# Performance work log

Hardware: AMD Instinct MI355X
Metric: run time of the kernel (lower is better)

Reference implementation:

```python
import jax, jax.numpy as jnp
import numpy as np

NUM_BINS = 256


def setup_inputs() -> dict:
    key = jax.random.key(0)
    x = jax.random.uniform(key, (16, 3, 1024, 1024), dtype=jnp.float32)
    return {"x": x}


def reference(x) -> jnp.ndarray:
    B, C, H, W = x.shape
    # Quantize to NUM_BINS levels (values in [0,1] so truncation == torch .long())
    x_flat = jnp.clip(x, 0.0, 1.0).reshape(B, C, H * W)
    x_q = jnp.clip((x_flat * (NUM_BINS - 1)).astype(jnp.int32), 0, NUM_BINS - 1)
    # Per-(B,C) histogram via a single flat scatter-add: offset each (b,c)
    # slice into its own NUM_BINS-wide segment of one 1-D buffer.
    offsets = (jnp.arange(B * C, dtype=jnp.int32) * NUM_BINS).reshape(B, C, 1)
    flat_idx = (x_q + offsets).reshape(-1)
    hist = jnp.zeros(B * C * NUM_BINS, dtype=jnp.float32).at[flat_idx].add(1.0)
    hist = hist.reshape(B, C, NUM_BINS)
    # CDF, normalized by total count (clamped at 1 to avoid div-by-zero)
    cdf = jnp.cumsum(hist, axis=2)
    cdf = cdf / jnp.maximum(cdf[:, :, -1:], 1.0)
    # Remap each pixel through its channel's CDF
    y_flat = jnp.take_along_axis(cdf, x_q, axis=2)
    return y_flat.reshape(B, C, H, W).astype(x.dtype)
```

## Files before the change

### kernel.cpp

```cpp
#include <hip/hip_runtime.h>

#define NB 256
#define NCH 48
#define HW (1024*1024)
#define WPC (HW / 4)
#define BPC 32
#define GRID (NCH * BPC)
#define THREADS 256
#define KTOT 32
#define KLDS 6
#define KREG (KTOT - KLDS)
#define FB_BPC 64

__device__ __forceinline__ int quant255(float v) {
    v = fminf(fmaxf(v, 0.0f), 1.0f);
    int q = (int)(v * 255.0f);
    q = q < 0 ? 0 : q;
    q = q > 255 ? 255 : q;
    return q;
}

__device__ __forceinline__ unsigned quant_pack(float4 v, unsigned* lh, int w) {
    int q0 = quant255(v.x), q1 = quant255(v.y);
    int q2 = quant255(v.z), q3 = quant255(v.w);
    atomicAdd(&lh[w * NB + q0], 1u);
    atomicAdd(&lh[w * NB + q1], 1u);
    atomicAdd(&lh[w * NB + q2], 1u);
    atomicAdd(&lh[w * NB + q3], 1u);
    return (unsigned)q0 | ((unsigned)q1 << 8)
         | ((unsigned)q2 << 16) | ((unsigned)q3 << 24);
}

__global__ __launch_bounds__(THREADS, 6) void fused_he_kernel(
    const float* __restrict__ x, unsigned int* __restrict__ ghist,
    unsigned int* __restrict__ bar, float* __restrict__ y) {
    __shared__ unsigned int sq[KLDS * THREADS];
    __shared__ unsigned int lh[4 * NB];

    const int t  = threadIdx.x;
    const int w  = t >> 6;
    const int ch  = blockIdx.x / BPC;
    const int blk = blockIdx.x % BPC;

    for (int i = t; i < 4 * NB; i += THREADS) lh[i] = 0u;
    __syncthreads();

    const float4* xp = (const float4*)x + (size_t)ch * WPC
                       + (size_t)blk * (KTOT * THREADS);

    for (int k = 0; k < KLDS; ++k) {
        float4 v = xp[k * THREADS + t];
        sq[k * THREADS + t] = quant_pack(v, lh, w);
    }
    unsigned int qpk[KREG];
    #pragma unroll
    for (int k = 0; k < KREG; ++k) {
        float4 v = xp[(KLDS + k) * THREADS + t];
        qpk[k] = quant_pack(v, lh, w);
    }
    __syncthreads();

    unsigned int s = lh[t] + lh[NB + t] + lh[2 * NB + t] + lh[3 * NB + t];
    atomicAdd(&ghist[ch * NB + t], s);
    __threadfence();
    __syncthreads();

    if (t == 0) {
        atomicAdd(bar, 1u);
        while (atomicAdd(bar, 0u) < (unsigned)GRID)
            __builtin_amdgcn_s_sleep(8);
    }
    __syncthreads();

    float* sbuf = (float*)lh;
    float* lut  = (float*)lh + NB;
    sbuf[t] = (float)atomicAdd(&ghist[ch * NB + t], 0u);
    __syncthreads();
    for (int off = 1; off < NB; off <<= 1) {
        float add = (t >= off) ? sbuf[t - off] : 0.0f;
        __syncthreads();
        sbuf[t] += add;
        __syncthreads();
    }
    float total = sbuf[NB - 1];
    lut[t] = sbuf[t] / fmaxf(total, 1.0f);
    __syncthreads();

    float4* yp = (float4*)y + (size_t)ch * WPC + (size_t)blk * (KTOT * THREADS);
    for (int k = 0; k < KLDS; ++k) {
        unsigned p = sq[k * THREADS + t];
        yp[k * THREADS + t] = make_float4(lut[p & 255], lut[(p >> 8) & 255],
                                          lut[(p >> 16) & 255], lut[p >> 24]);
    }
    #pragma unroll
    for (int k = 0; k < KREG; ++k) {
        unsigned p = qpk[k];
        yp[(KLDS + k) * THREADS + t] = make_float4(lut[p & 255], lut[(p >> 8) & 255],
                                                   lut[(p >> 16) & 255], lut[p >> 24]);
    }
}

__global__ __launch_bounds__(THREADS) void hist_quant_kernel(
    const float* __restrict__ x, unsigned int* __restrict__ ghist,
    unsigned int* __restrict__ q) {
    __shared__ unsigned int lh[4 * NB];
    const int t = threadIdx.x;
    const int w = t >> 6;
    for (int i = t; i < 4 * NB; i += THREADS) lh[i] = 0u;
    __syncthreads();

    const int ch  = blockIdx.x / FB_BPC;
    const int blk = blockIdx.x % FB_BPC;
    const float4* xp = (const float4*)(x + (size_t)ch * HW);
    unsigned int* qp = q + (size_t)ch * WPC;
    const int n4 = WPC / FB_BPC;
    const int base = blk * n4;

    for (int i = base + t; i < base + n4; i += THREADS) {
        float4 v = xp[i];
        qp[i] = quant_pack(v, lh, w);
    }
    __syncthreads();
    unsigned int s = lh[t] + lh[NB + t] + lh[2 * NB + t] + lh[3 * NB + t];
    if (s) atomicAdd(&ghist[ch * NB + t], s);
}

__global__ __launch_bounds__(THREADS) void cdf_remap_kernel(
    const unsigned int* __restrict__ q, const unsigned int* __restrict__ ghist,
    float* __restrict__ y) {
    __shared__ float sbuf[NB];
    __shared__ float lut[NB];
    const int t = threadIdx.x;
    const int ch  = blockIdx.x / FB_BPC;
    const int blk = blockIdx.x % FB_BPC;

    sbuf[t] = (float)ghist[ch * NB + t];
    __syncthreads();
    for (int off = 1; off < NB; off <<= 1) {
        float add = (t >= off) ? sbuf[t - off] : 0.0f;
        __syncthreads();
        sbuf[t] += add;
        __syncthreads();
    }
    float total = sbuf[NB - 1];
    lut[t] = sbuf[t] / fmaxf(total, 1.0f);
    __syncthreads();

    const unsigned int* qp = q + (size_t)ch * WPC;
    float4*             yp = (float4*)(y + (size_t)ch * HW);
    const int n4 = WPC / FB_BPC;
    const int base = blk * n4;
    for (int i = base + t; i < base + n4; i += THREADS) {
        unsigned p = qp[i];
        yp[i] = make_float4(lut[p & 255], lut[(p >> 8) & 255],
                            lut[(p >> 16) & 255], lut[p >> 24]);
    }
}

extern "C" void kernel_launch(void* const* d_in, const int* in_sizes, int n_in,
                              void* d_out, int out_size, void* d_ws, size_t ws_size,
                              hipStream_t stream) {
    const float* x = (const float*)d_in[0];
    float* y = (float*)d_out;

    unsigned int* ghist = (unsigned int*)d_ws;
    unsigned int* bar   = (unsigned int*)((char*)d_ws + 60 * 1024);
    unsigned int* q     = (unsigned int*)((char*)d_ws + 256 * 1024);

    hipMemsetAsync(d_ws, 0, 64 * 1024, stream);

    int occ = 0;
    hipError_t qe = hipOccupancyMaxActiveBlocksPerMultiprocessor(
        &occ, fused_he_kernel, THREADS, 0);
    bool fused_ok = (qe == hipSuccess) && (occ >= GRID / 256);

    if (fused_ok) {
        fused_he_kernel<<<GRID, THREADS, 0, stream>>>(x, ghist, bar, y);
    } else {
        hist_quant_kernel<<<NCH * FB_BPC, THREADS, 0, stream>>>(x, ghist, q);
        cdf_remap_kernel <<<NCH * FB_BPC, THREADS, 0, stream>>>(q, ghist, y);
    }
}
```

Before: 368.6 us.

## Replace persistent grid-barrier fused kernel with three-kernel histogram, LUT, remap pipeline

Removes the single fused kernel that kept quantized values in registers and LDS across a software grid barrier. It is replaced by three launches: histogram plus packed-quantize, a per-channel CDF/LUT build, and a remap that reads the packed bytes back from global memory. This drops the barrier spin and the occupancy dependence, and each remap block no longer recomputes the scan. The cost is an extra round trip of the packed quantized buffer through global memory and two more launches.

```diff
diff --git a/kernel.cpp b/kernel.cpp
--- a/kernel.cpp
+++ b/kernel.cpp
@@ -4,13 +4,10 @@
 #define NCH 48
 #define HW (1024*1024)
 #define WPC (HW / 4)
-#define BPC 32
-#define GRID (NCH * BPC)
 #define THREADS 256
-#define KTOT 32
-#define KLDS 6
-#define KREG (KTOT - KLDS)
-#define FB_BPC 64
+#define BPC 64
+#define N4 (WPC / BPC)
+
 
 __device__ __forceinline__ int quant255(float v) {
     v = fminf(fmaxf(v, 0.0f), 1.0f);
@@ -18,86 +15,6 @@
     q = q < 0 ? 0 : q;
     q = q > 255 ? 255 : q;
     return q;
-}
-
-__device__ __forceinline__ unsigned quant_pack(float4 v, unsigned* lh, int w) {
-    int q0 = quant255(v.x), q1 = quant255(v.y);
-    int q2 = quant255(v.z), q3 = quant255(v.w);
-    atomicAdd(&lh[w * NB + q0], 1u);
-    atomicAdd(&lh[w * NB + q1], 1u);
-    atomicAdd(&lh[w * NB + q2], 1u);
-    atomicAdd(&lh[w * NB + q3], 1u);
-    return (unsigned)q0 | ((unsigned)q1 << 8)
-         | ((unsigned)q2 << 16) | ((unsigned)q3 << 24);
-}
-
-__global__ __launch_bounds__(THREADS, 6) void fused_he_kernel(
-    const float* __restrict__ x, unsigned int* __restrict__ ghist,
-    unsigned int* __restrict__ bar, float* __restrict__ y) {
-    __shared__ unsigned int sq[KLDS * THREADS];
-    __shared__ unsigned int lh[4 * NB];
-
-    const int t  = threadIdx.x;
-    const int w  = t >> 6;
-    const int ch  = blockIdx.x / BPC;
-    const int blk = blockIdx.x % BPC;
-
-    for (int i = t; i < 4 * NB; i += THREADS) lh[i] = 0u;
-    __syncthreads();
-
-    const float4* xp = (const float4*)x + (size_t)ch * WPC
-                       + (size_t)blk * (KTOT * THREADS);
-
-    for (int k = 0; k < KLDS; ++k) {
-        float4 v = xp[k * THREADS + t];
-        sq[k * THREADS + t] = quant_pack(v, lh, w);
-    }
-    unsigned int qpk[KREG];
-    #pragma unroll
-    for (int k = 0; k < KREG; ++k) {
-        float4 v = xp[(KLDS + k) * THREADS + t];
-        qpk[k] = quant_pack(v, lh, w);
-    }
-    __syncthreads();
-
-    unsigned int s = lh[t] + lh[NB + t] + lh[2 * NB + t] + lh[3 * NB + t];
-    atomicAdd(&ghist[ch * NB + t], s);
-    __threadfence();
-    __syncthreads();
-
-    if (t == 0) {
-        atomicAdd(bar, 1u);
-        while (atomicAdd(bar, 0u) < (unsigned)GRID)
-            __builtin_amdgcn_s_sleep(8);
-    }
-    __syncthreads();
-
-    float* sbuf = (float*)lh;
-    float* lut  = (float*)lh + NB;
-    sbuf[t] = (float)atomicAdd(&ghist[ch * NB + t], 0u);
-    __syncthreads();
-    for (int off = 1; off < NB; off <<= 1) {
-        float add = (t >= off) ? sbuf[t - off] : 0.0f;
-        __syncthreads();
-        sbuf[t] += add;
-        __syncthreads();
-    }
-    float total = sbuf[NB - 1];
-    lut[t] = sbuf[t] / fmaxf(total, 1.0f);
-    __syncthreads();
-
-    float4* yp = (float4*)y + (size_t)ch * WPC + (size_t)blk * (KTOT * THREADS);
-    for (int k = 0; k < KLDS; ++k) {
-        unsigned p = sq[k * THREADS + t];
-        yp[k * THREADS + t] = make_float4(lut[p & 255], lut[(p >> 8) & 255],
-                                          lut[(p >> 16) & 255], lut[p >> 24]);
-    }
-    #pragma unroll
-    for (int k = 0; k < KREG; ++k) {
-        unsigned p = qpk[k];
-        yp[(KLDS + k) * THREADS + t] = make_float4(lut[p & 255], lut[(p >> 8) & 255],
-                                                   lut[(p >> 16) & 255], lut[p >> 24]);
-    }
 }
 
 __global__ __launch_bounds__(THREADS) void hist_quant_kernel(
@@ -109,31 +26,34 @@
     for (int i = t; i < 4 * NB; i += THREADS) lh[i] = 0u;
     __syncthreads();
 
-    const int ch  = blockIdx.x / FB_BPC;
-    const int blk = blockIdx.x % FB_BPC;
-    const float4* xp = (const float4*)(x + (size_t)ch * HW);
+    const int ch  = blockIdx.x / BPC;
+    const int blk = blockIdx.x % BPC;
+    const float4* xp = (const float4*)x + (size_t)ch * WPC;
     unsigned int* qp = q + (size_t)ch * WPC;
-    const int n4 = WPC / FB_BPC;
-    const int base = blk * n4;
+    const int base = blk * N4;
 
-    for (int i = base + t; i < base + n4; i += THREADS) {
+    #pragma unroll 4
+    for (int i = base + t; i < base + N4; i += THREADS) {
         float4 v = xp[i];
-        qp[i] = quant_pack(v, lh, w);
+        int q0 = quant255(v.x), q1 = quant255(v.y);
+        int q2 = quant255(v.z), q3 = quant255(v.w);
+        atomicAdd(&lh[w * NB + q0], 1u);
+        atomicAdd(&lh[w * NB + q1], 1u);
+        atomicAdd(&lh[w * NB + q2], 1u);
+        atomicAdd(&lh[w * NB + q3], 1u);
+        qp[i] = (unsigned)q0 | ((unsigned)q1 << 8)
+              | ((unsigned)q2 << 16) | ((unsigned)q3 << 24);
     }
     __syncthreads();
     unsigned int s = lh[t] + lh[NB + t] + lh[2 * NB + t] + lh[3 * NB + t];
     if (s) atomicAdd(&ghist[ch * NB + t], s);
 }
 
-__global__ __launch_bounds__(THREADS) void cdf_remap_kernel(
-    const unsigned int* __restrict__ q, const unsigned int* __restrict__ ghist,
-    float* __restrict__ y) {
+__global__ __launch_bounds__(THREADS) void lut_build_kernel(
+    const unsigned int* __restrict__ ghist, float* __restrict__ lutg) {
     __shared__ float sbuf[NB];
-    __shared__ float lut[NB];
-    const int t = threadIdx.x;
-    const int ch  = blockIdx.x / FB_BPC;
-    const int blk = blockIdx.x % FB_BPC;
-
+    const int t  = threadIdx.x;
+    const int ch = blockIdx.x;
     sbuf[t] = (float)ghist[ch * NB + t];
     __syncthreads();
     for (int off = 1; off < NB; off <<= 1) {
@@ -143,14 +63,26 @@
         __syncthreads();
     }
     float total = sbuf[NB - 1];
-    lut[t] = sbuf[t] / fmaxf(total, 1.0f);
+    lutg[ch * NB + t] = sbuf[t] / fmaxf(total, 1.0f);
+}
+
+__global__ __launch_bounds__(THREADS) void remap_kernel(
+    const unsigned int* __restrict__ q, const float* __restrict__ lutg,
+    float* __restrict__ y) {
+    __shared__ float lut[NB];
+    const int t   = threadIdx.x;
+    const int ch  = blockIdx.x / BPC;
+    const int blk = blockIdx.x % BPC;
+
+    lut[t] = lutg[ch * NB + t];
     __syncthreads();
 
     const unsigned int* qp = q + (size_t)ch * WPC;
-    float4*             yp = (float4*)(y + (size_t)ch * HW);
-    const int n4 = WPC / FB_BPC;
-    const int base = blk * n4;
-    for (int i = base + t; i < base + n4; i += THREADS) {
+    float4*             yp = (float4*)y + (size_t)ch * WPC;
+    const int base = blk * N4;
+
+    #pragma unroll 4
+    for (int i = base + t; i < base + N4; i += THREADS) {
         unsigned p = qp[i];
         yp[i] = make_float4(lut[p & 255], lut[(p >> 8) & 255],
                             lut[(p >> 16) & 255], lut[p >> 24]);
@@ -164,20 +96,12 @@
     float* y = (float*)d_out;
 
     unsigned int* ghist = (unsigned int*)d_ws;
-    unsigned int* bar   = (unsigned int*)((char*)d_ws + 60 * 1024);
+    float*        lutg  = (float*)((char*)d_ws + 64 * 1024);
     unsigned int* q     = (unsigned int*)((char*)d_ws + 256 * 1024);
 
-    hipMemsetAsync(d_ws, 0, 64 * 1024, stream);
+    hipMemsetAsync(d_ws, 0, 48 * 1024, stream);
 
-    int occ = 0;
-    hipError_t qe = hipOccupancyMaxActiveBlocksPerMultiprocessor(
-        &occ, fused_he_kernel, THREADS, 0);
-    bool fused_ok = (qe == hipSuccess) && (occ >= GRID / 256);
-
-    if (fused_ok) {
-        fused_he_kernel<<<GRID, THREADS, 0, stream>>>(x, ghist, bar, y);
-    } else {
-        hist_quant_kernel<<<NCH * FB_BPC, THREADS, 0, stream>>>(x, ghist, q);
-        cdf_remap_kernel <<<NCH * FB_BPC, THREADS, 0, stream>>>(q, ghist, y);
-    }
+    hist_quant_kernel<<<NCH * BPC, THREADS, 0, stream>>>(x, ghist, q);
+    lut_build_kernel <<<NCH,       THREADS, 0, stream>>>(ghist, lutg);
+    remap_kernel     <<<NCH * BPC, THREADS, 0, stream>>>(q, lutg, y);
 }
```

New measurement: 370.8 us. About the same (+0.6%).
